# Optimization experiments

Hardware: AMD Instinct MI355X
Metric: run time of the kernel (lower is better)

## Reference

```python
import jax, jax.numpy as jnp
import numpy as np

N, IN_DIM, OUT_DIM, HEADS = 4096, 128, 32, 4
EDGE_PROB = 0.015  # ~61 neighbors/node on average


def setup_inputs() -> dict:
    key = jax.random.key(0)
    k1, k2, k3, k4 = jax.random.split(key, 4)
    x = jax.random.normal(k1, (N, IN_DIM), dtype=jnp.float32)
    adj = (jax.random.uniform(k2, (N, N)) < EDGE_PROB).astype(jnp.float32)
    adj = jnp.maximum(adj, jnp.eye(N, dtype=jnp.float32))  # self loops so softmax is never all-masked
    # nn.Linear(in_dim, out_dim*heads, bias=False): weight stored here as [in, out]
    W = jax.random.normal(k3, (IN_DIM, OUT_DIM * HEADS), dtype=jnp.float32) / np.sqrt(IN_DIM).astype(np.float32)
    # nn.Linear(2*out_dim, 1, bias=False) -> a single [2*out_dim] vector shared across heads
    a = jax.random.normal(k4, (2 * OUT_DIM,), dtype=jnp.float32) / np.sqrt(2 * OUT_DIM).astype(np.float32)
    return {"x": x, "adj": adj, "W": W, "a": a}


def reference(x, adj, W, a):
    n = x.shape[0]
    xp = (x @ W).reshape(n, HEADS, OUT_DIM)  # [N, H, D]
    # Original builds concat([x_expanded, x_j_expanded])[i,j] = [x[j] || x[i]] and applies
    # a linear map. Since attn is linear, scores decompose: e[i,j,h] = a1.x[j,h] + a2.x[i,h].
    a_j, a_i = a[:OUT_DIM], a[OUT_DIM:]
    s_j = jnp.einsum('nhd,d->nh', xp, a_j)  # contribution of column node j
    s_i = jnp.einsum('nhd,d->nh', xp, a_i)  # contribution of row node i
    scale = jnp.float32(1.0 / np.sqrt(OUT_DIM))
    e = (s_i[:, None, :] + s_j[None, :, :]) * scale  # [N, N, H]
    e = e + ((1.0 - adj) * jnp.float32(-1e9))[:, :, None]
    att = jax.nn.softmax(e, axis=1)  # softmax over dim=1 (neighbors j), as in original
    out = jnp.einsum('ijh,jhd->ihd', att, xp)  # attention-weighted neighbor aggregation
    return out.reshape(n, HEADS * OUT_DIM)
```

## Files before the change

### kernel.cpp

```cpp
#include <hip/hip_runtime.h>

#define N_NODES 4096
#define IN_DIM  128
#define OUT_DIM 32
#define HEADS   4
#define FDIM    128
#define K1_ROWS 8
#define CAP     512

static __device__ __forceinline__ unsigned bf16pack(float a, float b) {
    unsigned ua = __float_as_uint(a), ub = __float_as_uint(b);
    ua = (ua + 0x7FFFu + ((ua >> 16) & 1u)) >> 16;
    ub = (ub + 0x7FFFu + ((ub >> 16) & 1u)) >> 16;
    return ua | (ub << 16);
}

__global__ __launch_bounds__(256) void gat_proj(const float* __restrict__ x,
                                                const float* __restrict__ W,
                                                const float* __restrict__ a,
                                                unsigned* __restrict__ Ybf,
                                                float* __restrict__ Eg) {
    __shared__ float xs[K1_ROWS * IN_DIM];
    __shared__ float eS[K1_ROWS][HEADS];
    const int t    = threadIdx.x;
    const int row0 = blockIdx.x * K1_ROWS;

    ((float4*)xs)[t] = ((const float4*)(x + (size_t)row0 * IN_DIM))[t];
    __syncthreads();

    const int c  = t & 127;
    const int rg = t >> 7;
    const float* xb = xs + (rg * 4) * IN_DIM;

    float acc0 = 0.f, acc1 = 0.f, acc2 = 0.f, acc3 = 0.f;
#pragma unroll 4
    for (int k0 = 0; k0 < IN_DIM; k0 += 4) {
        const float w0 = W[(k0 + 0) * FDIM + c];
        const float w1 = W[(k0 + 1) * FDIM + c];
        const float w2 = W[(k0 + 2) * FDIM + c];
        const float w3 = W[(k0 + 3) * FDIM + c];
        const float4 x0 = *(const float4*)(xb + 0 * IN_DIM + k0);
        const float4 x1 = *(const float4*)(xb + 1 * IN_DIM + k0);
        const float4 x2 = *(const float4*)(xb + 2 * IN_DIM + k0);
        const float4 x3 = *(const float4*)(xb + 3 * IN_DIM + k0);
        acc0 = fmaf(x0.x, w0, fmaf(x0.y, w1, fmaf(x0.z, w2, fmaf(x0.w, w3, acc0))));
        acc1 = fmaf(x1.x, w0, fmaf(x1.y, w1, fmaf(x1.z, w2, fmaf(x1.w, w3, acc1))));
        acc2 = fmaf(x2.x, w0, fmaf(x2.y, w1, fmaf(x2.z, w2, fmaf(x2.w, w3, acc2))));
        acc3 = fmaf(x3.x, w0, fmaf(x3.y, w1, fmaf(x3.z, w2, fmaf(x3.w, w3, acc3))));
    }

    const int rb = rg * 4;
    __syncthreads();
    xs[(rb + 0) * FDIM + c] = acc0;
    xs[(rb + 1) * FDIM + c] = acc1;
    xs[(rb + 2) * FDIM + c] = acc2;
    xs[(rb + 3) * FDIM + c] = acc3;
    __syncthreads();

    if (t < K1_ROWS * HEADS) {
        const int r = t >> 2, h = t & 3;
        const float4* xr = (const float4*)(xs + r * FDIM + h * OUT_DIM);
        const float4* aj = (const float4*)a;
        float vj = 0.f;
#pragma unroll
        for (int q = 0; q < 8; ++q) {
            const float4 xv = xr[q], a0 = aj[q];
            vj += xv.x * a0.x + xv.y * a0.y + xv.z * a0.z + xv.w * a0.w;
        }
        const float e = __expf(vj * 0.17677669529663687f);
        eS[r][h] = e;
        Eg[(row0 + r) * HEADS + h] = e;
    }
    __syncthreads();

#pragma unroll
    for (int q = 0; q < 2; ++q) {
        const int idx = t + 256 * q;
        const int r   = idx >> 6;
        const int cp  = idx & 63;
        const float e = eS[r][cp >> 4];
        const float a0 = xs[r * FDIM + 2 * cp]     * e;
        const float a1 = xs[r * FDIM + 2 * cp + 1] * e;
        Ybf[(size_t)(row0 + r) * 64 + cp] = bf16pack(a0, a1);
    }
}

__global__ __launch_bounds__(256, 6) void gat_sum(const float* __restrict__ adj,
                                                  const unsigned* __restrict__ Ybf,
                                                  const float* __restrict__ E,
                                                  float* __restrict__ out) {
    const int tid  = threadIdx.x;
    const int wv   = tid >> 6;
    const int lane = tid & 63;
    const int row  = blockIdx.x * 2 + (wv >> 1);
    const int half = wv & 1;
    const int hm   = lane >> 4;

    __shared__ int    seg_s[4][CAP];
    __shared__ float4 part_s[4][64];

    const float4* arow = (const float4*)(adj + (size_t)row * N_NODES) + half * 512;
    float4 v[8];
#pragma unroll
    for (int c = 0; c < 8; ++c) v[c] = arow[c * 64 + lane];

    const unsigned long long lt = (1ULL << lane) - 1ULL;
    int* seg = seg_s[wv];
    int base = 0;
#pragma unroll
    for (int c = 0; c < 8; ++c) {
        const int cb = half * 2048 + c * 256 + lane * 4;
        const float vals[4] = {v[c].x, v[c].y, v[c].z, v[c].w};
#pragma unroll
        for (int m = 0; m < 4; ++m) {
            const unsigned long long mk = __ballot(vals[m] != 0.f);
            const int pos = base + __popcll(mk & lt);
            if (vals[m] != 0.f && pos < CAP) seg[pos] = cb + m;
            base += __popcll(mk);
        }
    }
    const int cnt = base;

    const float* Eh = E + hm;
    float ax0 = 0.f, ay0 = 0.f, z0 = 0.f;
    float ax1 = 0.f, ay1 = 0.f, z1 = 0.f;
    float ax2 = 0.f, ay2 = 0.f, z2 = 0.f;
    float ax3 = 0.f, ay3 = 0.f, z3 = 0.f;

#define ACC(ch, u, ev)                                                        \
    {                                                                         \
        ax##ch += __uint_as_float((u) << 16);                                 \
        ay##ch += __uint_as_float((u) & 0xFFFF0000u);                         \
        z##ch  += (ev);                                                       \
    }

    if (__builtin_expect(cnt <= CAP, 1)) {
        int e = 0;
        for (; e + 16 <= cnt; e += 16) {
            const int4 ja = *(const int4*)&seg[e];
            const int4 jb = *(const int4*)&seg[e + 4];
            const int4 jc = *(const int4*)&seg[e + 8];
            const int4 jd = *(const int4*)&seg[e + 12];
            const unsigned u0  = Ybf[(size_t)ja.x * 64 + lane];
            const unsigned u1  = Ybf[(size_t)ja.y * 64 + lane];
            const unsigned u2  = Ybf[(size_t)ja.z * 64 + lane];
            const unsigned u3  = Ybf[(size_t)ja.w * 64 + lane];
            const unsigned u4  = Ybf[(size_t)jb.x * 64 + lane];
            const unsigned u5  = Ybf[(size_t)jb.y * 64 + lane];
            const unsigned u6  = Ybf[(size_t)jb.z * 64 + lane];
            const unsigned u7  = Ybf[(size_t)jb.w * 64 + lane];
            const unsigned u8  = Ybf[(size_t)jc.x * 64 + lane];
            const unsigned u9  = Ybf[(size_t)jc.y * 64 + lane];
            const unsigned u10 = Ybf[(size_t)jc.z * 64 + lane];
            const unsigned u11 = Ybf[(size_t)jc.w * 64 + lane];
            const unsigned u12 = Ybf[(size_t)jd.x * 64 + lane];
            const unsigned u13 = Ybf[(size_t)jd.y * 64 + lane];
            const unsigned u14 = Ybf[(size_t)jd.z * 64 + lane];
            const unsigned u15 = Ybf[(size_t)jd.w * 64 + lane];
            const float e0  = Eh[(size_t)ja.x * 4];
            const float e1  = Eh[(size_t)ja.y * 4];
            const float e2  = Eh[(size_t)ja.z * 4];
            const float e3  = Eh[(size_t)ja.w * 4];
            const float e4  = Eh[(size_t)jb.x * 4];
            const float e5  = Eh[(size_t)jb.y * 4];
            const float e6  = Eh[(size_t)jb.z * 4];
            const float e7  = Eh[(size_t)jb.w * 4];
            const float e8  = Eh[(size_t)jc.x * 4];
            const float e9  = Eh[(size_t)jc.y * 4];
            const float e10 = Eh[(size_t)jc.z * 4];
            const float e11 = Eh[(size_t)jc.w * 4];
            const float e12 = Eh[(size_t)jd.x * 4];
            const float e13 = Eh[(size_t)jd.y * 4];
            const float e14 = Eh[(size_t)jd.z * 4];
            const float e15 = Eh[(size_t)jd.w * 4];
            ACC(0, u0,  e0)  ACC(1, u1,  e1)  ACC(2, u2,  e2)  ACC(3, u3,  e3)
            ACC(0, u4,  e4)  ACC(1, u5,  e5)  ACC(2, u6,  e6)  ACC(3, u7,  e7)
            ACC(0, u8,  e8)  ACC(1, u9,  e9)  ACC(2, u10, e10) ACC(3, u11, e11)
            ACC(0, u12, e12) ACC(1, u13, e13) ACC(2, u14, e14) ACC(3, u15, e15)
        }
        for (; e + 4 <= cnt; e += 4) {
            const int4 ja = *(const int4*)&seg[e];
            const unsigned u0 = Ybf[(size_t)ja.x * 64 + lane];
            const unsigned u1 = Ybf[(size_t)ja.y * 64 + lane];
            const unsigned u2 = Ybf[(size_t)ja.z * 64 + lane];
            const unsigned u3 = Ybf[(size_t)ja.w * 64 + lane];
            const float e0 = Eh[(size_t)ja.x * 4];
            const float e1 = Eh[(size_t)ja.y * 4];
            const float e2 = Eh[(size_t)ja.z * 4];
            const float e3 = Eh[(size_t)ja.w * 4];
            ACC(0, u0, e0) ACC(1, u1, e1) ACC(2, u2, e2) ACC(3, u3, e3)
        }
        for (; e < cnt; ++e) {
            const int j = seg[e];
            const unsigned u = Ybf[(size_t)j * 64 + lane];
            ACC(0, u, Eh[(size_t)j * 4])
        }
    } else {
#pragma unroll
        for (int c = 0; c < 8; ++c) {
            const float vals[4] = {v[c].x, v[c].y, v[c].z, v[c].w};
#pragma unroll
            for (int m = 0; m < 4; ++m) {
                unsigned long long mask = __ballot(vals[m] != 0.f);
                while (mask) {
                    const int b = __builtin_ctzll(mask);
                    mask &= mask - 1ULL;
                    const int j = half * 2048 + c * 256 + b * 4 + m;
                    const unsigned u = Ybf[(size_t)j * 64 + lane];
                    ACC(0, u, Eh[(size_t)j * 4])
                }
            }
        }
    }
#undef ACC

    part_s[wv][lane] = make_float4((ax0 + ax1) + (ax2 + ax3),
                                   (ay0 + ay1) + (ay2 + ay3),
                                   (z0 + z1) + (z2 + z3), 0.f);
    __syncthreads();

    if ((wv & 1) == 0) {
        const float4 pa = part_s[wv][lane];
        const float4 pb = part_s[wv + 1][lane];
        const float invZ = 1.0f / (pa.z + pb.z);
        float2 o;
        o.x = (pa.x + pb.x) * invZ;
        o.y = (pa.y + pb.y) * invZ;
        ((float2*)out)[(size_t)row * 64 + lane] = o;
    }
}

extern "C" void kernel_launch(void* const* d_in, const int* in_sizes, int n_in,
                              void* d_out, int out_size, void* d_ws, size_t ws_size,
                              hipStream_t stream) {
    const float* x   = (const float*)d_in[0];
    const float* adj = (const float*)d_in[1];
    const float* W   = (const float*)d_in[2];
    const float* a   = (const float*)d_in[3];
    float* out = (float*)d_out;

    unsigned* Ybf = (unsigned*)d_ws;
    float*    E   = (float*)(Ybf + (size_t)N_NODES * 64);

    gat_proj<<<N_NODES / K1_ROWS, 256, 0, stream>>>(x, W, a, Ybf, E);
    gat_sum<<<N_NODES / 2, 256, 0, stream>>>(adj, Ybf, E, out);
}
```

Measured before the change: 29.47 us.

## Split wave into two half-waves gathering alternate neighbors with 8-byte loads

The gather loop now has each 32-lane half of a wave handle alternating neighbors. Each lane loads a uint2 (four bf16 features) instead of one unsigned, which doubles the number of neighbors in flight per wave instruction. The halves are merged with a cross-lane shuffle before the existing block-level reduction. The CAP is cut to 192 and the launch bounds are raised to 8 blocks per CU, trading LDS and registers for occupancy. Rows with more than 192 neighbors fall back to the slower ballot path.

New measurement: 28.27 us. 1.04x faster.

```diff
diff --git a/kernel.cpp b/kernel.cpp
--- a/kernel.cpp
+++ b/kernel.cpp
@@ -6,7 +6,7 @@
 #define HEADS   4
 #define FDIM    128
 #define K1_ROWS 8
-#define CAP     512
+#define CAP     192
 
 static __device__ __forceinline__ unsigned bf16pack(float a, float b) {
     unsigned ua = __float_as_uint(a), ub = __float_as_uint(b);
@@ -85,7 +85,7 @@
     }
 }
 
-__global__ __launch_bounds__(256, 6) void gat_sum(const float* __restrict__ adj,
+__global__ __launch_bounds__(256, 8) void gat_sum(const float* __restrict__ adj,
                                                   const unsigned* __restrict__ Ybf,
                                                   const float* __restrict__ E,
                                                   float* __restrict__ out) {
@@ -94,10 +94,13 @@
     const int lane = tid & 63;
     const int row  = blockIdx.x * 2 + (wv >> 1);
     const int half = wv & 1;
-    const int hm   = lane >> 4;
+    const int ll   = lane & 31;
+    const int sel  = lane >> 5;
+    const int hm8  = ll >> 3;
 
     __shared__ int    seg_s[4][CAP];
-    __shared__ float4 part_s[4][64];
+    __shared__ float4 partv[4][32];
+    __shared__ float  partz[4][32];
 
     const float4* arow = (const float4*)(adj + (size_t)row * N_NODES) + half * 512;
     float4 v[8];
@@ -121,81 +124,64 @@
     }
     const int cnt = base;
 
-    const float* Eh = E + hm;
-    float ax0 = 0.f, ay0 = 0.f, z0 = 0.f;
-    float ax1 = 0.f, ay1 = 0.f, z1 = 0.f;
-    float ax2 = 0.f, ay2 = 0.f, z2 = 0.f;
-    float ax3 = 0.f, ay3 = 0.f, z3 = 0.f;
-
-#define ACC(ch, u, ev)                                                        \
+    const uint2* Y2 = (const uint2*)Ybf;
+    float a0 = 0.f, a1 = 0.f, a2 = 0.f, a3 = 0.f, za = 0.f;
+    float b0 = 0.f, b1 = 0.f, b2 = 0.f, b3 = 0.f, zb = 0.f;
+
+#define ACCA(u, ev)                                                           \
     {                                                                         \
-        ax##ch += __uint_as_float((u) << 16);                                 \
-        ay##ch += __uint_as_float((u) & 0xFFFF0000u);                         \
-        z##ch  += (ev);                                                       \
+        a0 += __uint_as_float((u).x << 16);                                   \
+        a1 += __uint_as_float((u).x & 0xFFFF0000u);                           \
+        a2 += __uint_as_float((u).y << 16);                                   \
+        a3 += __uint_as_float((u).y & 0xFFFF0000u);                           \
+        za += (ev);                                                           \
+    }
+#define ACCB(u, ev)                                                           \
+    {                                                                         \
+        b0 += __uint_as_float((u).x << 16);                                   \
+        b1 += __uint_as_float((u).x & 0xFFFF0000u);                           \
+        b2 += __uint_as_float((u).y << 16);                                   \
+        b3 += __uint_as_float((u).y & 0xFFFF0000u);                           \
+        zb += (ev);                                                           \
     }
 
     if (__builtin_expect(cnt <= CAP, 1)) {
-        int e = 0;
-        for (; e + 16 <= cnt; e += 16) {
-            const int4 ja = *(const int4*)&seg[e];
-            const int4 jb = *(const int4*)&seg[e + 4];
-            const int4 jc = *(const int4*)&seg[e + 8];
-            const int4 jd = *(const int4*)&seg[e + 12];
-            const unsigned u0  = Ybf[(size_t)ja.x * 64 + lane];
-            const unsigned u1  = Ybf[(size_t)ja.y * 64 + lane];
-            const unsigned u2  = Ybf[(size_t)ja.z * 64 + lane];
-            const unsigned u3  = Ybf[(size_t)ja.w * 64 + lane];
-            const unsigned u4  = Ybf[(size_t)jb.x * 64 + lane];
-            const unsigned u5  = Ybf[(size_t)jb.y * 64 + lane];
-            const unsigned u6  = Ybf[(size_t)jb.z * 64 + lane];
-            const unsigned u7  = Ybf[(size_t)jb.w * 64 + lane];
-            const unsigned u8  = Ybf[(size_t)jc.x * 64 + lane];
-            const unsigned u9  = Ybf[(size_t)jc.y * 64 + lane];
-            const unsigned u10 = Ybf[(size_t)jc.z * 64 + lane];
-            const unsigned u11 = Ybf[(size_t)jc.w * 64 + lane];
-            const unsigned u12 = Ybf[(size_t)jd.x * 64 + lane];
-            const unsigned u13 = Ybf[(size_t)jd.y * 64 + lane];
-            const unsigned u14 = Ybf[(size_t)jd.z * 64 + lane];
-            const unsigned u15 = Ybf[(size_t)jd.w * 64 + lane];
-            const float e0  = Eh[(size_t)ja.x * 4];
-            const float e1  = Eh[(size_t)ja.y * 4];
-            const float e2  = Eh[(size_t)ja.z * 4];
-            const float e3  = Eh[(size_t)ja.w * 4];
-            const float e4  = Eh[(size_t)jb.x * 4];
-            const float e5  = Eh[(size_t)jb.y * 4];
-            const float e6  = Eh[(size_t)jb.z * 4];
-            const float e7  = Eh[(size_t)jb.w * 4];
-            const float e8  = Eh[(size_t)jc.x * 4];
-            const float e9  = Eh[(size_t)jc.y * 4];
-            const float e10 = Eh[(size_t)jc.z * 4];
-            const float e11 = Eh[(size_t)jc.w * 4];
-            const float e12 = Eh[(size_t)jd.x * 4];
-            const float e13 = Eh[(size_t)jd.y * 4];
-            const float e14 = Eh[(size_t)jd.z * 4];
-            const float e15 = Eh[(size_t)jd.w * 4];
-            ACC(0, u0,  e0)  ACC(1, u1,  e1)  ACC(2, u2,  e2)  ACC(3, u3,  e3)
-            ACC(0, u4,  e4)  ACC(1, u5,  e5)  ACC(2, u6,  e6)  ACC(3, u7,  e7)
-            ACC(0, u8,  e8)  ACC(1, u9,  e9)  ACC(2, u10, e10) ACC(3, u11, e11)
-            ACC(0, u12, e12) ACC(1, u13, e13) ACC(2, u14, e14) ACC(3, u15, e15)
-        }
-        for (; e + 4 <= cnt; e += 4) {
-            const int4 ja = *(const int4*)&seg[e];
-            const unsigned u0 = Ybf[(size_t)ja.x * 64 + lane];
-            const unsigned u1 = Ybf[(size_t)ja.y * 64 + lane];
-            const unsigned u2 = Ybf[(size_t)ja.z * 64 + lane];
-            const unsigned u3 = Ybf[(size_t)ja.w * 64 + lane];
-            const float e0 = Eh[(size_t)ja.x * 4];
-            const float e1 = Eh[(size_t)ja.y * 4];
-            const float e2 = Eh[(size_t)ja.z * 4];
-            const float e3 = Eh[(size_t)ja.w * 4];
-            ACC(0, u0, e0) ACC(1, u1, e1) ACC(2, u2, e2) ACC(3, u3, e3)
-        }
-        for (; e < cnt; ++e) {
-            const int j = seg[e];
-            const unsigned u = Ybf[(size_t)j * 64 + lane];
-            ACC(0, u, Eh[(size_t)j * 4])
+        const int npair = cnt >> 1;
+        int p = 0;
+        for (; p + 4 <= npair; p += 4) {
+            const int4 q0 = *(const int4*)&seg[2 * p];
+            const int4 q1 = *(const int4*)&seg[2 * p + 4];
+            const int j0 = sel ? q0.y : q0.x;
+            const int j1 = sel ? q0.w : q0.z;
+            const int j2 = sel ? q1.y : q1.x;
+            const int j3 = sel ? q1.w : q1.z;
+            const uint2 y0 = Y2[(size_t)j0 * 32 + ll];
+            const uint2 y1 = Y2[(size_t)j1 * 32 + ll];
+            const uint2 y2 = Y2[(size_t)j2 * 32 + ll];
+            const uint2 y3 = Y2[(size_t)j3 * 32 + ll];
+            const float e0 = E[(size_t)j0 * 4 + hm8];
+            const float e1 = E[(size_t)j1 * 4 + hm8];
+            const float e2 = E[(size_t)j2 * 4 + hm8];
+            const float e3 = E[(size_t)j3 * 4 + hm8];
+            ACCA(y0, e0) ACCB(y1, e1) ACCA(y2, e2) ACCB(y3, e3)
+        }
+        for (; p < npair; ++p) {
+            const int2 q = *(const int2*)&seg[2 * p];
+            const int j = sel ? q.y : q.x;
+            const uint2 y = Y2[(size_t)j * 32 + ll];
+            const float e = E[(size_t)j * 4 + hm8];
+            ACCA(y, e)
+        }
+        if (cnt & 1) {
+            const int j = seg[cnt - 1];
+            if (sel == 0) {
+                const uint2 y = Y2[(size_t)j * 32 + ll];
+                const float e = E[(size_t)j * 4 + hm8];
+                ACCA(y, e)
+            }
         }
     } else {
+        int ep = 0;
 #pragma unroll
         for (int c = 0; c < 8; ++c) {
             const float vals[4] = {v[c].x, v[c].y, v[c].z, v[c].w};
@@ -205,28 +191,43 @@
                 while (mask) {
                     const int b = __builtin_ctzll(mask);
                     mask &= mask - 1ULL;
-                    const int j = half * 2048 + c * 256 + b * 4 + m;
-                    const unsigned u = Ybf[(size_t)j * 64 + lane];
-                    ACC(0, u, Eh[(size_t)j * 4])
+                    if ((ep & 1) == sel) {
+                        const int j = half * 2048 + c * 256 + b * 4 + m;
+                        const uint2 y = Y2[(size_t)j * 32 + ll];
+                        const float e = E[(size_t)j * 4 + hm8];
+                        ACCA(y, e)
+                    }
+                    ++ep;
                 }
             }
         }
     }
-#undef ACC
-
-    part_s[wv][lane] = make_float4((ax0 + ax1) + (ax2 + ax3),
-                                   (ay0 + ay1) + (ay2 + ay3),
-                                   (z0 + z1) + (z2 + z3), 0.f);
-    __syncthreads();
-
-    if ((wv & 1) == 0) {
-        const float4 pa = part_s[wv][lane];
-        const float4 pb = part_s[wv + 1][lane];
-        const float invZ = 1.0f / (pa.z + pb.z);
-        float2 o;
+#undef ACCA
+#undef ACCB
+
+    a0 += b0; a1 += b1; a2 += b2; a3 += b3; za += zb;
+    a0 += __shfl_down(a0, 32);
+    a1 += __shfl_down(a1, 32);
+    a2 += __shfl_down(a2, 32);
+    a3 += __shfl_down(a3, 32);
+    za += __shfl_down(za, 32);
+
+    if (lane < 32) {
+        partv[wv][ll] = make_float4(a0, a1, a2, a3);
+        partz[wv][ll] = za;
+    }
+    __syncthreads();
+
+    if ((wv & 1) == 0 && lane < 32) {
+        const float4 pa = partv[wv][ll];
+        const float4 pb = partv[wv + 1][ll];
+        const float invZ = 1.0f / (partz[wv][ll] + partz[wv + 1][ll]);
+        float4 o;
         o.x = (pa.x + pb.x) * invZ;
         o.y = (pa.y + pb.y) * invZ;
-        ((float2*)out)[(size_t)row * 64 + lane] = o;
+        o.z = (pa.z + pb.z) * invZ;
+        o.w = (pa.w + pb.w) * invZ;
+        ((float4*)out)[(size_t)row * 32 + ll] = o;
     }
 }
 
```
